# Performance work log

Measured on AMD Instinct MI355X. Metric: run time of the kernel, lower is better.

## Reference

```python
import jax, jax.numpy as jnp
import numpy as np

EMBED_DIM = 1024
NUM_HEADS = 16
HEAD_DIM = EMBED_DIM // NUM_HEADS
SEQ = 2048
BATCH = 2


def setup_inputs() -> dict:
    key = jax.random.key(0)
    ks = jax.random.split(key, 8)
    s = 1.0 / np.sqrt(EMBED_DIM)
    return {
        "query": jax.random.normal(ks[0], (SEQ, BATCH, EMBED_DIM), jnp.float32),
        "key": jax.random.normal(ks[1], (SEQ, BATCH, EMBED_DIM), jnp.float32),
        "value": jax.random.normal(ks[2], (SEQ, BATCH, EMBED_DIM), jnp.float32),
        "Wq": jax.random.normal(ks[3], (EMBED_DIM, EMBED_DIM), jnp.float32) * s,
        "Wk": jax.random.normal(ks[4], (EMBED_DIM, EMBED_DIM), jnp.float32) * s,
        "Wv": jax.random.normal(ks[5], (EMBED_DIM, EMBED_DIM), jnp.float32) * s,
        "in_bias": jnp.zeros((3 * EMBED_DIM,), jnp.float32),
        "Wo": jax.random.normal(ks[6], (EMBED_DIM, EMBED_DIM), jnp.float32) * s,
        "bo": jnp.zeros((EMBED_DIM,), jnp.float32),
    }


def reference(query, key, value, Wq, Wk, Wv, in_bias, Wo, bo):
    E, H, D = EMBED_DIM, NUM_HEADS, HEAD_DIM
    # seq-first -> batch-first: [T,B,E] -> [B,T,E]
    q_in = jnp.transpose(query, (1, 0, 2))
    k_in = jnp.transpose(key, (1, 0, 2))
    v_in = jnp.transpose(value, (1, 0, 2))
    B, T, _ = q_in.shape

    # fused in-projection (torch _in_projection: x @ W.T + b)
    q = q_in @ Wq.T + in_bias[:E]
    k = k_in @ Wk.T + in_bias[E:2 * E]
    v = v_in @ Wv.T + in_bias[2 * E:]

    # split heads: [B,T,E] -> [B,H,T,D]
    def split_heads(x):
        return jnp.transpose(x.reshape(B, T, H, D), (0, 2, 1, 3))

    q, k, v = split_heads(q), split_heads(k), split_heads(v)

    # multi-linear (causal linear) attention with outer-product KV state:
    # kv_store[b,h,t] = sum_{s<=t} k_s (outer) v_s        -> [B,H,T,D,D]
    kv_store = jnp.cumsum(jnp.einsum("bhtk,bhtv->bhtkv", k, v), axis=2)
    scale = 1.0 / np.sqrt(D)
    attn = jnp.einsum("bhtk,bhtkv->bhtv", q, kv_store) * scale  # [B,H,T,D]

    # merge heads + out projection
    out = jnp.transpose(attn, (0, 2, 1, 3)).reshape(B, T, E)
    out = out @ Wo.T + bo
    # batch-first -> seq-first
    return jnp.transpose(out, (1, 0, 2))
```

## Files before the change

kernel.cpp:

```cpp
#include <hip/hip_runtime.h>


#define TSEQ 2048
#define BBATCH 2
#define EE 1024
#define TOK 4096
#define NCH 32

typedef _Float16 half8 __attribute__((ext_vector_type(8)));
typedef _Float16 half4 __attribute__((ext_vector_type(4)));
typedef float f32x4 __attribute__((ext_vector_type(4)));

#ifndef __has_builtin
#define __has_builtin(x) 0
#endif
#if __has_builtin(__builtin_amdgcn_global_load_lds)
#define USE_GLL 1
#endif

#ifdef USE_GLL
typedef __attribute__((address_space(1))) const unsigned int guint_t;
typedef __attribute__((address_space(3))) unsigned int luint_t;
#endif

__global__ __launch_bounds__(256) void pack_x_kernel(
    const float* __restrict__ q, const float* __restrict__ k,
    const float* __restrict__ v,
    _Float16* __restrict__ xq, _Float16* __restrict__ xk,
    _Float16* __restrict__ xv) {
  const int blk = blockIdx.x;
  const int m = blk >> 12;
  const int row = blk & 4095;
  const int b = row >> 11, t = row & 2047;
  const float* src = (m == 0 ? q : (m == 1 ? k : v)) +
                     (size_t)t * (BBATCH * EE) + (size_t)b * EE;
  _Float16* dst = (m == 0 ? xq : (m == 1 ? xk : xv)) + (size_t)row * EE;
  const int e = threadIdx.x * 4;
  f32x4 f = *(const f32x4*)&src[e];
  half4 h;
  h[0] = (_Float16)f[0]; h[1] = (_Float16)f[1];
  h[2] = (_Float16)f[2]; h[3] = (_Float16)f[3];
  *(half4*)&dst[e] = h;
}

__global__ __launch_bounds__(256) void pack_w_kernel(
    const float* __restrict__ wq, const float* __restrict__ wk,
    const float* __restrict__ wv, const float* __restrict__ wo,
    _Float16* __restrict__ wb) {
  const int blk = blockIdx.x;
  const int m = blk >> 10, row = blk & 1023;
  const float* src =
      (m == 0 ? wq : (m == 1 ? wk : (m == 2 ? wv : wo))) + (size_t)row * EE;
  _Float16* dst = wb + (size_t)m * EE * EE + (size_t)row * EE;
  const int e = threadIdx.x * 4;
  f32x4 f = *(const f32x4*)&src[e];
  half4 h;
  h[0] = (_Float16)f[0]; h[1] = (_Float16)f[1];
  h[2] = (_Float16)f[2]; h[3] = (_Float16)f[3];
  *(half4*)&dst[e] = h;
}

__device__ __forceinline__ void stage_tile(
    const _Float16* __restrict__ A, const _Float16* __restrict__ Bm,
    long arow0, long brow0, int k0, int tid, int w,
    _Float16* __restrict__ Ab, _Float16* __restrict__ Bb) {
#pragma unroll
  for (int i = 0; i < 4; ++i) {
    const int flat = i * 256 + tid;
    const int r = flat >> 3, c = (flat & 7) * 8;
    const _Float16* ga = &A[(size_t)(arow0 + r) * 1024 + k0 + c];
    const _Float16* gb = &Bm[(size_t)(brow0 + r) * 1024 + k0 + c];
#ifdef USE_GLL
    const int ubase = (i * 256 + w * 64) * 8;
    __builtin_amdgcn_global_load_lds((guint_t*)ga, (luint_t*)&Ab[ubase], 16, 0,
                                     0);
    __builtin_amdgcn_global_load_lds((guint_t*)gb, (luint_t*)&Bb[ubase], 16, 0,
                                     0);
#else
    *(half8*)&Ab[flat * 8] = *(const half8*)ga;
    *(half8*)&Bb[flat * 8] = *(const half8*)gb;
#endif
  }
}

__device__ __forceinline__ void gemm_core(
    const _Float16* __restrict__ A, const _Float16* __restrict__ Bm,
    long arow0, long brow0, int tid, f32x4 (&acc)[4][4],
    _Float16 (&Ab)[2][8192], _Float16 (&Bb)[2][8192]) {
  const int lane = tid & 63, w = tid >> 6;
  const int wr = w >> 1, wc = w & 1;
  const int l15 = lane & 15, lg = lane >> 4;

#ifdef USE_GLL
  stage_tile(A, Bm, arow0, brow0, 0, tid, w, Ab[0], Bb[0]);
  for (int kt = 0; kt < 16; ++kt) {
    const int cur = kt & 1;
    if (kt < 15) {
      stage_tile(A, Bm, arow0, brow0, (kt + 1) * 64, tid, w, Ab[cur ^ 1],
                 Bb[cur ^ 1]);
      asm volatile("s_waitcnt vmcnt(8)" ::: "memory");
    } else {
      asm volatile("s_waitcnt vmcnt(0)" ::: "memory");
    }
    __builtin_amdgcn_s_barrier();
    asm volatile("" ::: "memory");
#pragma unroll
    for (int ks = 0; ks < 2; ++ks) {
      half8 af[4], bf[4];
#pragma unroll
      for (int mi = 0; mi < 4; ++mi)
        af[mi] = *(const half8*)&Ab[cur][(wr * 64 + mi * 16 + l15) * 64 +
                                         ks * 32 + lg * 8];
#pragma unroll
      for (int ni = 0; ni < 4; ++ni)
        bf[ni] = *(const half8*)&Bb[cur][(wc * 64 + ni * 16 + l15) * 64 +
                                         ks * 32 + lg * 8];
#pragma unroll
      for (int mi = 0; mi < 4; ++mi)
#pragma unroll
        for (int ni = 0; ni < 4; ++ni)
          acc[mi][ni] = __builtin_amdgcn_mfma_f32_16x16x32_f16(
              af[mi], bf[ni], acc[mi][ni], 0, 0, 0);
    }
    asm volatile("" ::: "memory");
    __builtin_amdgcn_s_barrier();
  }
#else
  for (int kt = 0; kt < 16; ++kt) {
    __syncthreads();
    stage_tile(A, Bm, arow0, brow0, kt * 64, tid, w, Ab[0], Bb[0]);
    __syncthreads();
#pragma unroll
    for (int ks = 0; ks < 2; ++ks) {
      half8 af[4], bf[4];
#pragma unroll
      for (int mi = 0; mi < 4; ++mi)
        af[mi] = *(const half8*)&Ab[0][(wr * 64 + mi * 16 + l15) * 64 +
                                       ks * 32 + lg * 8];
#pragma unroll
      for (int ni = 0; ni < 4; ++ni)
        bf[ni] = *(const half8*)&Bb[0][(wc * 64 + ni * 16 + l15) * 64 +
                                       ks * 32 + lg * 8];
#pragma unroll
      for (int mi = 0; mi < 4; ++mi)
#pragma unroll
        for (int ni = 0; ni < 4; ++ni)
          acc[mi][ni] = __builtin_amdgcn_mfma_f32_16x16x32_f16(
              af[mi], bf[ni], acc[mi][ni], 0, 0, 0);
    }
  }
#endif
}

__global__ __launch_bounds__(256) void gemm_inproj(
    const _Float16* __restrict__ X, const _Float16* __restrict__ WB,
    const float* __restrict__ bias, _Float16* __restrict__ Qb,
    _Float16* __restrict__ Kbf, _Float16* __restrict__ KT,
    _Float16* __restrict__ VT) {
  __shared__ __align__(16) _Float16 Ab[2][8192];
  __shared__ __align__(16) _Float16 Bb[2][8192];
  const int tid = threadIdx.x;
  const int which = blockIdx.x >> 3;
  const long arow0 = (long)blockIdx.y * 128;
  const long brow0 = (long)(blockIdx.x & 7) * 128;
  const _Float16* A = X + (size_t)which * (TOK * EE);
  const _Float16* Bm = WB + (size_t)which * (EE * EE);
  const float* bs = bias + which * EE;

  f32x4 acc[4][4] = {};
  gemm_core(A, Bm, arow0, brow0, tid, acc, Ab, Bb);

  const int lane = tid & 63, w = tid >> 6;
  const int wr = w >> 1, wc = w & 1;
  const int l15 = lane & 15, lg = lane >> 4;
#pragma unroll
  for (int mi = 0; mi < 4; ++mi) {
#pragma unroll
    for (int ni = 0; ni < 4; ++ni) {
      const long gm = arow0 + wr * 64 + mi * 16 + lg * 4;
      const long gn = brow0 + wc * 64 + ni * 16 + l15;
      const float bv = bs[gn];
      float vv[4];
#pragma unroll
      for (int r = 0; r < 4; ++r) vv[r] = acc[mi][ni][r] + bv;
      if (which == 0) {
#pragma unroll
        for (int r = 0; r < 4; ++r)
          Qb[(size_t)(gm + r) * EE + gn] = (_Float16)vv[r];
      } else if (which == 1) {
#pragma unroll
        for (int r = 0; r < 4; ++r)
          Kbf[(size_t)(gm + r) * EE + gn] = (_Float16)vv[r];
        half4 pk;
#pragma unroll
        for (int r = 0; r < 4; ++r) pk[r] = (_Float16)vv[r];
        *(half4*)&KT[(size_t)gn * TOK + gm] = pk;
      } else {
        half4 pk;
#pragma unroll
        for (int r = 0; r < 4; ++r) pk[r] = (_Float16)vv[r];
        *(half4*)&VT[(size_t)gn * TOK + gm] = pk;
      }
    }
  }
}

__global__ __launch_bounds__(256) void gemm_out(
    const _Float16* __restrict__ Wo, const _Float16* __restrict__ ATT,
    const float* __restrict__ bo, float* __restrict__ OF) {
  __shared__ __align__(16) _Float16 Ab[2][8192];
  __shared__ __align__(16) _Float16 Bb[2][8192];
  const int tid = threadIdx.x;
  const long arow0 = (long)blockIdx.y * 128;
  const long brow0 = (long)blockIdx.x * 128;

  f32x4 acc[4][4] = {};
  gemm_core(Wo, ATT, arow0, brow0, tid, acc, Ab, Bb);

  const int lane = tid & 63, w = tid >> 6;
  const int wr = w >> 1, wc = w & 1;
  const int l15 = lane & 15, lg = lane >> 4;
#pragma unroll
  for (int mi = 0; mi < 4; ++mi) {
#pragma unroll
    for (int ni = 0; ni < 4; ++ni) {
      const long gm = arow0 + wr * 64 + mi * 16 + lg * 4;
      const long gn = brow0 + wc * 64 + ni * 16 + l15;
      const int t = (int)(gn & 2047), b2 = (int)(gn >> 11);
      f32x4 res;
#pragma unroll
      for (int r = 0; r < 4; ++r) res[r] = acc[mi][ni][r] + bo[gm + r];
      *(f32x4*)&OF[(size_t)t * (BBATCH * EE) + (size_t)b2 * EE + gm] = res;
    }
  }
}

__global__ __launch_bounds__(64) void chunk_g_kernel(
    const _Float16* __restrict__ KT, const _Float16* __restrict__ VT,
    _Float16* __restrict__ GT) {
  const int c = blockIdx.x & 31, bh = blockIdx.x >> 5;
  const int b = bh >> 4, h = bh & 15;
  const int lane = threadIdx.x, l15 = lane & 15, lg = lane >> 4;
  const long tok0 = (long)b * TSEQ + c * 64;

  half8 af[4][2], bf[4][2];
#pragma unroll
  for (int ma = 0; ma < 4; ++ma)
#pragma unroll
    for (int ks = 0; ks < 2; ++ks) {
      const size_t rowoff = (size_t)(h * 64 + ma * 16 + l15) * TOK + tok0 +
                            ks * 32 + lg * 8;
      af[ma][ks] = *(const half8*)&KT[rowoff];
      bf[ma][ks] = *(const half8*)&VT[rowoff];
    }
  f32x4 acc[4][4] = {};
#pragma unroll
  for (int ks = 0; ks < 2; ++ks)
#pragma unroll
    for (int ma = 0; ma < 4; ++ma)
#pragma unroll
      for (int nb = 0; nb < 4; ++nb)
        acc[ma][nb] = __builtin_amdgcn_mfma_f32_16x16x32_f16(
            af[ma][ks], bf[nb][ks], acc[ma][nb], 0, 0, 0);
  _Float16* g = GT + ((size_t)bh * NCH + c) * 4096;
#pragma unroll
  for (int ma = 0; ma < 4; ++ma)
#pragma unroll
    for (int nb = 0; nb < 4; ++nb) {
      half4 pk;
#pragma unroll
      for (int r = 0; r < 4; ++r) pk[r] = (_Float16)acc[ma][nb][r];
      *(half4*)&g[(nb * 16 + l15) * 64 + ma * 16 + lg * 4] = pk;
    }
}

__global__ __launch_bounds__(256) void scan_kernel(
    const _Float16* __restrict__ GT, _Float16* __restrict__ ST) {
  const int gid = blockIdx.x * 256 + threadIdx.x;
  const int bh = gid >> 12, el = gid & 4095;
  const size_t base = (size_t)bh * NCH * 4096 + el;
  float acc = 0.f;
  for (int c = 0; c < NCH; ++c) {
    ST[base + (size_t)c * 4096] = (_Float16)acc;
    acc += (float)GT[base + (size_t)c * 4096];
  }
}

__global__ __launch_bounds__(64) void attn_chunk_kernel(
    const _Float16* __restrict__ Q, const _Float16* __restrict__ Kb,
    const _Float16* __restrict__ VT, const _Float16* __restrict__ ST,
    _Float16* __restrict__ attn) {
  __shared__ __align__(16) _Float16 sc[64 * 72];
  const int c = blockIdx.x & 31, bh = blockIdx.x >> 5;
  const int b = bh >> 4, h = bh & 15;
  const int lane = threadIdx.x, l15 = lane & 15, lg = lane >> 4;
  const long tok0 = (long)b * TSEQ + c * 64;

  half8 qb[4][2];
#pragma unroll
  for (int nb = 0; nb < 4; ++nb)
#pragma unroll
    for (int ks = 0; ks < 2; ++ks)
      qb[nb][ks] = *(const half8*)&Q[(size_t)(tok0 + nb * 16 + l15) * EE +
                                     h * 64 + ks * 32 + lg * 8];

  f32x4 sT[4][4] = {};
#pragma unroll
  for (int ks = 0; ks < 2; ++ks) {
    half8 kf[4];
#pragma unroll
    for (int ma = 0; ma < 4; ++ma)
      kf[ma] = *(const half8*)&Kb[(size_t)(tok0 + ma * 16 + l15) * EE +
                                  h * 64 + ks * 32 + lg * 8];
#pragma unroll
    for (int ma = 0; ma < 4; ++ma)
#pragma unroll
      for (int nb = 0; nb < 4; ++nb)
        sT[ma][nb] = __builtin_amdgcn_mfma_f32_16x16x32_f16(
            kf[ma], qb[nb][ks], sT[ma][nb], 0, 0, 0);
  }
#pragma unroll
  for (int ma = 0; ma < 4; ++ma)
#pragma unroll
    for (int nb = 0; nb < 4; ++nb) {
      const int tp0 = ma * 16 + lg * 4, t = nb * 16 + l15;
      half4 pk;
#pragma unroll
      for (int r = 0; r < 4; ++r)
        pk[r] = (tp0 + r <= t) ? (_Float16)sT[ma][nb][r] : (_Float16)0.f;
      *(half4*)&sc[t * 72 + tp0] = pk;
    }
  __syncthreads();

  f32x4 o[4][4] = {};
  const _Float16* st = ST + ((size_t)bh * NCH + c) * 4096;
#pragma unroll
  for (int ks = 0; ks < 2; ++ks) {
    half8 sf[4];
#pragma unroll
    for (int ma = 0; ma < 4; ++ma)
      sf[ma] = *(const half8*)&st[(ma * 16 + l15) * 64 + ks * 32 + lg * 8];
#pragma unroll
    for (int ma = 0; ma < 4; ++ma)
#pragma unroll
      for (int nb = 0; nb < 4; ++nb)
        o[ma][nb] = __builtin_amdgcn_mfma_f32_16x16x32_f16(
            sf[ma], qb[nb][ks], o[ma][nb], 0, 0, 0);
  }
#pragma unroll
  for (int ks = 0; ks < 2; ++ks) {
    half8 vf[4], sb[4];
#pragma unroll
    for (int ma = 0; ma < 4; ++ma)
      vf[ma] = *(const half8*)&VT[(size_t)(h * 64 + ma * 16 + l15) * TOK +
                                  tok0 + ks * 32 + lg * 8];
#pragma unroll
    for (int nb = 0; nb < 4; ++nb)
      sb[nb] = *(const half8*)&sc[(nb * 16 + l15) * 72 + ks * 32 + lg * 8];
#pragma unroll
    for (int ma = 0; ma < 4; ++ma)
#pragma unroll
      for (int nb = 0; nb < 4; ++nb)
        o[ma][nb] = __builtin_amdgcn_mfma_f32_16x16x32_f16(
            vf[ma], sb[nb], o[ma][nb], 0, 0, 0);
  }
#pragma unroll
  for (int ma = 0; ma < 4; ++ma)
#pragma unroll
    for (int nb = 0; nb < 4; ++nb) {
      const int t = nb * 16 + l15, d20 = ma * 16 + lg * 4;
      half4 pk;
#pragma unroll
      for (int r = 0; r < 4; ++r) pk[r] = (_Float16)(o[ma][nb][r] * 0.125f);
      *(half4*)&attn[(size_t)(tok0 + t) * EE + h * 64 + d20] = pk;
    }
}

extern "C" void kernel_launch(void* const* d_in, const int* in_sizes, int n_in,
                              void* d_out, int out_size, void* d_ws,
                              size_t ws_size, hipStream_t stream) {
  const float* q = (const float*)d_in[0];
  const float* k = (const float*)d_in[1];
  const float* v = (const float*)d_in[2];
  const float* Wq = (const float*)d_in[3];
  const float* Wk = (const float*)d_in[4];
  const float* Wv = (const float*)d_in[5];
  const float* in_bias = (const float*)d_in[6];
  const float* Wo = (const float*)d_in[7];
  const float* bo = (const float*)d_in[8];
  float* out = (float*)d_out;

  char* ws = (char*)d_ws;
  const size_t MB = 1u << 20;
  _Float16* wb = (_Float16*)(ws + 0 * MB);
  _Float16* xq = (_Float16*)(ws + 8 * MB);
  _Float16* xk = (_Float16*)(ws + 16 * MB);
  _Float16* xv = (_Float16*)(ws + 24 * MB);
  _Float16* Qb = (_Float16*)(ws + 32 * MB);
  _Float16* Kbf = (_Float16*)(ws + 40 * MB);
  _Float16* KT = (_Float16*)(ws + 48 * MB);
  _Float16* VT = (_Float16*)(ws + 56 * MB);
  _Float16* attnb = (_Float16*)(ws + 8 * MB);
  _Float16* GT = (_Float16*)(ws + 16 * MB);
  _Float16* STb = (_Float16*)(ws + 24 * MB);

  pack_x_kernel<<<12288, 256, 0, stream>>>(q, k, v, xq, xk, xv);
  pack_w_kernel<<<4096, 256, 0, stream>>>(Wq, Wk, Wv, Wo, wb);

  dim3 gi(24, 32);
  gemm_inproj<<<gi, 256, 0, stream>>>(xq, wb, in_bias, Qb, Kbf, KT, VT);

  chunk_g_kernel<<<1024, 64, 0, stream>>>(KT, VT, GT);
  scan_kernel<<<512, 256, 0, stream>>>(GT, STb);
  attn_chunk_kernel<<<1024, 64, 0, stream>>>(Qb, Kbf, VT, STb, attnb);

  dim3 go(32, 8);
  gemm_out<<<go, 256, 0, stream>>>(wb + 3145728, attnb, bo, out);
}
```

Baseline: 220.7 us.

## Restructure GEMM main loop into triple-buffered K=32 stages with swizzled LDS

The shared GEMM core moves from double-buffered 64-wide K tiles to triple-buffered 32-wide K tiles, prefetching two stages ahead with a single barrier per step. An XOR swizzle on LDS slots is meant to cut bank conflicts, and sched_barriers pin the instruction order. Grid indices are remapped from 2D to a 1D logical order that groups blocks for L2 and XCD locality, and launch bounds request three blocks per CU. In exchange it doubles the number of loop iterations and barriers, and it relies on exact vmcnt accounting to stay correct.

```diff
diff --git a/kernel.cpp b/kernel.cpp
--- a/kernel.cpp
+++ b/kernel.cpp
@@ -60,18 +60,19 @@
   *(half4*)&dst[e] = h;
 }
 
-__device__ __forceinline__ void stage_tile(
+__device__ __forceinline__ void stage32(
     const _Float16* __restrict__ A, const _Float16* __restrict__ Bm,
     long arow0, long brow0, int k0, int tid, int w,
     _Float16* __restrict__ Ab, _Float16* __restrict__ Bb) {
 #pragma unroll
-  for (int i = 0; i < 4; ++i) {
-    const int flat = i * 256 + tid;
-    const int r = flat >> 3, c = (flat & 7) * 8;
+  for (int rnd = 0; rnd < 2; ++rnd) {
+    const int flat = rnd * 256 + tid;
+    const int r = flat >> 2, s = flat & 3;
+    const int c = (s ^ ((r >> 1) & 3)) * 8;
     const _Float16* ga = &A[(size_t)(arow0 + r) * 1024 + k0 + c];
     const _Float16* gb = &Bm[(size_t)(brow0 + r) * 1024 + k0 + c];
 #ifdef USE_GLL
-    const int ubase = (i * 256 + w * 64) * 8;
+    const int ubase = (rnd * 256 + w * 64) * 8;
     __builtin_amdgcn_global_load_lds((guint_t*)ga, (luint_t*)&Ab[ubase], 16, 0,
                                      0);
     __builtin_amdgcn_global_load_lds((guint_t*)gb, (luint_t*)&Bb[ubase], 16, 0,
@@ -83,92 +84,94 @@
   }
 }
 
-__device__ __forceinline__ void gemm_core(
+__device__ __forceinline__ void gemm_core32(
     const _Float16* __restrict__ A, const _Float16* __restrict__ Bm,
     long arow0, long brow0, int tid, f32x4 (&acc)[4][4],
-    _Float16 (&Ab)[2][8192], _Float16 (&Bb)[2][8192]) {
+    _Float16 (&Ab)[3][4096], _Float16 (&Bb)[3][4096]) {
   const int lane = tid & 63, w = tid >> 6;
   const int wr = w >> 1, wc = w & 1;
   const int l15 = lane & 15, lg = lane >> 4;
+  const int slotx = (l15 >> 1) & 3;
 
 #ifdef USE_GLL
-  stage_tile(A, Bm, arow0, brow0, 0, tid, w, Ab[0], Bb[0]);
-  for (int kt = 0; kt < 16; ++kt) {
-    const int cur = kt & 1;
-    if (kt < 15) {
-      stage_tile(A, Bm, arow0, brow0, (kt + 1) * 64, tid, w, Ab[cur ^ 1],
-                 Bb[cur ^ 1]);
-      asm volatile("s_waitcnt vmcnt(8)" ::: "memory");
-    } else {
+  stage32(A, Bm, arow0, brow0, 0, tid, w, Ab[0], Bb[0]);
+  stage32(A, Bm, arow0, brow0, 32, tid, w, Ab[1], Bb[1]);
+  asm volatile("s_waitcnt vmcnt(4)" ::: "memory");
+  __builtin_amdgcn_s_barrier();
+  int cur = 0, nxt2 = 2;
+  for (int T = 0; T < 32; ++T) {
+    __builtin_amdgcn_sched_barrier(0);
+    if (T + 2 < 32)
+      stage32(A, Bm, arow0, brow0, (T + 2) * 32, tid, w, Ab[nxt2], Bb[nxt2]);
+    half8 af[4], bf[4];
+#pragma unroll
+    for (int mi = 0; mi < 4; ++mi)
+      af[mi] = *(const half8*)&Ab[cur][(wr * 64 + mi * 16 + l15) * 32 +
+                                       ((lg ^ slotx) * 8)];
+#pragma unroll
+    for (int ni = 0; ni < 4; ++ni)
+      bf[ni] = *(const half8*)&Bb[cur][(wc * 64 + ni * 16 + l15) * 32 +
+                                       ((lg ^ slotx) * 8)];
+#pragma unroll
+    for (int mi = 0; mi < 4; ++mi)
+#pragma unroll
+      for (int ni = 0; ni < 4; ++ni)
+        acc[mi][ni] = __builtin_amdgcn_mfma_f32_16x16x32_f16(
+            af[mi], bf[ni], acc[mi][ni], 0, 0, 0);
+    __builtin_amdgcn_sched_barrier(0);
+    if (T < 30) {
+      asm volatile("s_waitcnt vmcnt(4)" ::: "memory");
+    } else if (T == 30) {
       asm volatile("s_waitcnt vmcnt(0)" ::: "memory");
     }
-    __builtin_amdgcn_s_barrier();
-    asm volatile("" ::: "memory");
-#pragma unroll
-    for (int ks = 0; ks < 2; ++ks) {
-      half8 af[4], bf[4];
-#pragma unroll
-      for (int mi = 0; mi < 4; ++mi)
-        af[mi] = *(const half8*)&Ab[cur][(wr * 64 + mi * 16 + l15) * 64 +
-                                         ks * 32 + lg * 8];
+    if (T < 31) __builtin_amdgcn_s_barrier();
+    cur = (cur == 2) ? 0 : cur + 1;
+    nxt2 = (nxt2 == 2) ? 0 : nxt2 + 1;
+  }
+#else
+  for (int T = 0; T < 32; ++T) {
+    __syncthreads();
+    stage32(A, Bm, arow0, brow0, T * 32, tid, w, Ab[0], Bb[0]);
+    __syncthreads();
+    half8 af[4], bf[4];
+#pragma unroll
+    for (int mi = 0; mi < 4; ++mi)
+      af[mi] = *(const half8*)&Ab[0][(wr * 64 + mi * 16 + l15) * 32 +
+                                     ((lg ^ slotx) * 8)];
+#pragma unroll
+    for (int ni = 0; ni < 4; ++ni)
+      bf[ni] = *(const half8*)&Bb[0][(wc * 64 + ni * 16 + l15) * 32 +
+                                     ((lg ^ slotx) * 8)];
+#pragma unroll
+    for (int mi = 0; mi < 4; ++mi)
 #pragma unroll
       for (int ni = 0; ni < 4; ++ni)
-        bf[ni] = *(const half8*)&Bb[cur][(wc * 64 + ni * 16 + l15) * 64 +
-                                         ks * 32 + lg * 8];
-#pragma unroll
-      for (int mi = 0; mi < 4; ++mi)
-#pragma unroll
-        for (int ni = 0; ni < 4; ++ni)
-          acc[mi][ni] = __builtin_amdgcn_mfma_f32_16x16x32_f16(
-              af[mi], bf[ni], acc[mi][ni], 0, 0, 0);
-    }
-    asm volatile("" ::: "memory");
-    __builtin_amdgcn_s_barrier();
-  }
-#else
-  for (int kt = 0; kt < 16; ++kt) {
-    __syncthreads();
-    stage_tile(A, Bm, arow0, brow0, kt * 64, tid, w, Ab[0], Bb[0]);
-    __syncthreads();
-#pragma unroll
-    for (int ks = 0; ks < 2; ++ks) {
-      half8 af[4], bf[4];
-#pragma unroll
-      for (int mi = 0; mi < 4; ++mi)
-        af[mi] = *(const half8*)&Ab[0][(wr * 64 + mi * 16 + l15) * 64 +
-                                       ks * 32 + lg * 8];
-#pragma unroll
-      for (int ni = 0; ni < 4; ++ni)
-        bf[ni] = *(const half8*)&Bb[0][(wc * 64 + ni * 16 + l15) * 64 +
-                                       ks * 32 + lg * 8];
-#pragma unroll
-      for (int mi = 0; mi < 4; ++mi)
-#pragma unroll
-        for (int ni = 0; ni < 4; ++ni)
-          acc[mi][ni] = __builtin_amdgcn_mfma_f32_16x16x32_f16(
-              af[mi], bf[ni], acc[mi][ni], 0, 0, 0);
-    }
+        acc[mi][ni] = __builtin_amdgcn_mfma_f32_16x16x32_f16(
+            af[mi], bf[ni], acc[mi][ni], 0, 0, 0);
   }
 #endif
 }
 
-__global__ __launch_bounds__(256) void gemm_inproj(
+__global__ __launch_bounds__(256, 3) void gemm_inproj(
     const _Float16* __restrict__ X, const _Float16* __restrict__ WB,
     const float* __restrict__ bias, _Float16* __restrict__ Qb,
     _Float16* __restrict__ Kbf, _Float16* __restrict__ KT,
     _Float16* __restrict__ VT) {
-  __shared__ __align__(16) _Float16 Ab[2][8192];
-  __shared__ __align__(16) _Float16 Bb[2][8192];
+  __shared__ __align__(16) _Float16 Ab[3][4096];
+  __shared__ __align__(16) _Float16 Bb[3][4096];
   const int tid = threadIdx.x;
-  const int which = blockIdx.x >> 3;
-  const long arow0 = (long)blockIdx.y * 128;
-  const long brow0 = (long)(blockIdx.x & 7) * 128;
+  const int logical = (blockIdx.x & 7) * 96 + (blockIdx.x >> 3);
+  const int mb = logical / 24;
+  const int col = logical % 24;
+  const int which = col >> 3, nb = col & 7;
+  const long arow0 = (long)mb * 128;
+  const long brow0 = (long)nb * 128;
   const _Float16* A = X + (size_t)which * (TOK * EE);
   const _Float16* Bm = WB + (size_t)which * (EE * EE);
   const float* bs = bias + which * EE;
 
   f32x4 acc[4][4] = {};
-  gemm_core(A, Bm, arow0, brow0, tid, acc, Ab, Bb);
+  gemm_core32(A, Bm, arow0, brow0, tid, acc, Ab, Bb);
 
   const int lane = tid & 63, w = tid >> 6;
   const int wr = w >> 1, wc = w & 1;
@@ -205,17 +208,20 @@
   }
 }
 
-__global__ __launch_bounds__(256) void gemm_out(
+__global__ __launch_bounds__(256, 3) void gemm_out(
     const _Float16* __restrict__ Wo, const _Float16* __restrict__ ATT,
     const float* __restrict__ bo, float* __restrict__ OF) {
-  __shared__ __align__(16) _Float16 Ab[2][8192];
-  __shared__ __align__(16) _Float16 Bb[2][8192];
+  __shared__ __align__(16) _Float16 Ab[3][4096];
+  __shared__ __align__(16) _Float16 Bb[3][4096];
   const int tid = threadIdx.x;
-  const long arow0 = (long)blockIdx.y * 128;
-  const long brow0 = (long)blockIdx.x * 128;
+  const int logical = (blockIdx.x & 7) * 32 + (blockIdx.x >> 3);
+  const int mb = logical >> 5;
+  const int col = logical & 31;
+  const long arow0 = (long)mb * 128;
+  const long brow0 = (long)col * 128;
 
   f32x4 acc[4][4] = {};
-  gemm_core(Wo, ATT, arow0, brow0, tid, acc, Ab, Bb);
+  gemm_core32(Wo, ATT, arow0, brow0, tid, acc, Ab, Bb);
 
   const int lane = tid & 63, w = tid >> 6;
   const int wr = w >> 1, wc = w & 1;
@@ -407,13 +413,11 @@
   pack_x_kernel<<<12288, 256, 0, stream>>>(q, k, v, xq, xk, xv);
   pack_w_kernel<<<4096, 256, 0, stream>>>(Wq, Wk, Wv, Wo, wb);
 
-  dim3 gi(24, 32);
-  gemm_inproj<<<gi, 256, 0, stream>>>(xq, wb, in_bias, Qb, Kbf, KT, VT);
+  gemm_inproj<<<768, 256, 0, stream>>>(xq, wb, in_bias, Qb, Kbf, KT, VT);
 
   chunk_g_kernel<<<1024, 64, 0, stream>>>(KT, VT, GT);
   scan_kernel<<<512, 256, 0, stream>>>(GT, STb);
   attn_chunk_kernel<<<1024, 64, 0, stream>>>(Qb, Kbf, VT, STb, attnb);
 
-  dim3 go(32, 8);
-  gemm_out<<<go, 256, 0, stream>>>(wb + 3145728, attnb, bo, out);
-}
+  gemm_out<<<256, 256, 0, stream>>>(wb + 3145728, attnb, bo, out);
+}
```

Result: faster. 199.9 us (-9.5%).
